# Kernel optimization log

Hardware: AMD Instinct MI355X
Metric: run time of the kernel (lower is better)

## Reference

```python
import jax, jax.numpy as jnp
import numpy as np

N_ING, N_DIR = 100000, 50000
E = 1000000
H, D = 4, 16          # heads, per-head dim
HID = H * D           # 64
LAT, COND = 32, 8
F_ING, F_DIR = 16, 8
OUT_ING = 16


def _han_edge(x_src, x_dst, att_s, att_d, edge_index, n_dst):
    # HANConv per-edge-type attention message passing.
    src, dst = edge_index[0], edge_index[1]
    a = jax.nn.leaky_relu(
        jnp.einsum('nhd,hd->nh', x_src, att_s)[src]
        + jnp.einsum('nhd,hd->nh', x_dst, att_d)[dst],
        negative_slope=0.2)                               # [E, H]
    amax = jax.ops.segment_max(a, dst, num_segments=n_dst)
    ex = jnp.exp(a - amax[dst])
    denom = jax.ops.segment_sum(ex, dst, num_segments=n_dst)
    alpha = ex / (denom[dst] + 1e-16)                     # PyG softmax eps
    out = jax.ops.segment_sum(x_src[src] * alpha[:, :, None], dst,
                              num_segments=n_dst)         # [n_dst, H, D]
    return jax.nn.relu(out.reshape(n_dst, HID))


def _group(outs, q, Wk, bk):
    # HANConv semantic-level attention across edge types.
    s = jnp.stack(outs)                                   # [T, N, HID]
    score = jnp.tanh(s @ Wk + bk).mean(axis=1) @ q        # [T]
    attn = jax.nn.softmax(score)
    return jnp.einsum('t,tnf->nf', attn, s)


def setup_inputs() -> dict:
    key = jax.random.key(0)
    ks = jax.random.split(key, 32)
    def ei(k, n_src, n_dst):
        k1, k2 = jax.random.split(k)
        return jnp.stack([jax.random.randint(k1, (E,), 0, n_src),
                          jax.random.randint(k2, (E,), 0, n_dst)]).astype(jnp.int64)
    s = 0.1
    inp = {
        'x_ing': jax.random.normal(ks[0], (N_ING, F_ING), jnp.float32),
        'x_dir': jax.random.normal(ks[1], (N_DIR, F_DIR), jnp.float32),
        'cond':  jax.random.normal(ks[2], (COND,), jnp.float32),
        'eps':   jax.random.normal(ks[3], (1, LAT), jnp.float32),
        'ei_cooc':     ei(ks[4], N_ING, N_DIR),
        'ei_used':     ei(ks[5], N_ING, N_DIR),
        'ei_contains': ei(ks[6], N_DIR, N_ING),
        'ei_pairs':    ei(ks[7], N_DIR, N_DIR),
        'ei_follows':  ei(ks[8], N_DIR, N_DIR),
        # node-type projections
        'W_pi': jax.random.normal(ks[9],  (F_ING, HID)) * s,
        'b_pi': jnp.zeros((HID,)),
        'W_pd': jax.random.normal(ks[10], (F_DIR, HID)) * s,
        'b_pd': jnp.zeros((HID,)),
        # semantic attention
        'Wk': jax.random.normal(ks[21], (HID, HID)) * s,
        'bk': jnp.zeros((HID,)),
        'q':  jax.random.normal(ks[22], (HID,)) * s,
        # VAE heads (input: 2*HID + COND)
        'W_mu': jax.random.normal(ks[23], (2 * HID + COND, LAT)) * s,
        'b_mu': jnp.zeros((LAT,)),
        'W_lv': jax.random.normal(ks[24], (2 * HID + COND, LAT)) * s,
        'b_lv': jnp.zeros((LAT,)),
        # decoder (fc1 is dead code in the original forward)
        'W_fc3': jax.random.normal(ks[25], (LAT, HID)) * s,
        'b_fc3': jnp.zeros((HID,)),
        'W_fc2': jax.random.normal(ks[26], (HID, OUT_ING)) * s,
        'b_fc2': jnp.zeros((OUT_ING,)),
    }
    for i, name in enumerate(['cooc', 'used', 'contains', 'pairs', 'follows']):
        inp[f'as_{name}'] = jax.random.normal(ks[11 + i], (H, D)) * s
        inp[f'ad_{name}'] = jax.random.normal(ks[16 + i], (H, D)) * s
    return inp


def reference(x_ing, x_dir, cond, eps,
              ei_cooc, ei_used, ei_contains, ei_pairs, ei_follows,
              W_pi, b_pi, W_pd, b_pd,
              as_cooc, ad_cooc, as_used, ad_used, as_contains, ad_contains,
              as_pairs, ad_pairs, as_follows, ad_follows,
              Wk, bk, q, W_mu, b_mu, W_lv, b_lv,
              W_fc3, b_fc3, W_fc2, b_fc2):
    # node-type projections -> [N, H, D]
    h_ing = (x_ing @ W_pi + b_pi).reshape(N_ING, H, D)
    h_dir = (x_dir @ W_pd + b_pd).reshape(N_DIR, H, D)

    o_cooc = _han_edge(h_ing, h_dir, as_cooc, ad_cooc, ei_cooc, N_DIR)
    o_used = _han_edge(h_ing, h_dir, as_used, ad_used, ei_used, N_DIR)
    o_cont = _han_edge(h_dir, h_ing, as_contains, ad_contains, ei_contains, N_ING)
    o_pair = _han_edge(h_dir, h_dir, as_pairs, ad_pairs, ei_pairs, N_DIR)
    o_foll = _han_edge(h_dir, h_dir, as_follows, ad_follows, ei_follows, N_DIR)

    out_ing = _group([o_cont], q, Wk, bk)                       # [N_ING, HID]
    out_dir = _group([o_cooc, o_used, o_pair, o_foll], q, Wk, bk)

    ingre_pool = out_ing.mean(axis=0, keepdims=True)            # [1, HID]
    direc_pool = out_dir.mean(axis=0, keepdims=True)
    graph_repr = jnp.concatenate([ingre_pool, direc_pool, cond[None]], axis=1)

    mu = graph_repr @ W_mu + b_mu
    logvar = graph_repr @ W_lv + b_lv
    z = mu + eps * jnp.exp(0.5 * logvar)

    # decoder: fc1 branch is overwritten in the original; effective path below
    recon = jnp.tanh(jax.nn.relu(z @ W_fc3 + b_fc3) @ W_fc2 + b_fc2)  # [1, OUT_ING]
    return recon, mu, logvar
```

## Files before the change

### kernel.cpp

```cpp
#include <hip/hip_runtime.h>
#include <hip/hip_fp16.h>
#include <math.h>

#define N_ING 100000
#define N_DIR 50000
#define NE    1000000
#define NDST_TOTAL 300000
#define NBUCK 4688
#define BA    64
#define NBK   (5 * BA)
#define I4PT  (NE / 4)
#define PB_ING 384
#define PB_DIR 192
#define LOG2E 1.442695041f

typedef float v2f __attribute__((ext_vector_type(2)));
typedef __attribute__((ext_vector_type(8))) short bf16x8;
typedef __attribute__((ext_vector_type(4))) float f32x4;

__global__ __launch_bounds__(256) void kA_kernel(
    const int* __restrict__ e0, const int* __restrict__ e1,
    const int* __restrict__ e2, const int* __restrict__ e3,
    const int* __restrict__ e4, int* __restrict__ blockcnt,
    const float* __restrict__ x_ing, const float* __restrict__ W_pi,
    const float* __restrict__ b_pi,
    const float* __restrict__ as_cooc, const float* __restrict__ as_used,
    const float* __restrict__ ad_contains,
    unsigned* __restrict__ h8_ing, __half* __restrict__ s_ing,
    const float* __restrict__ x_dir, const float* __restrict__ W_pd,
    const float* __restrict__ b_pd,
    const float* __restrict__ ad_cooc, const float* __restrict__ ad_used,
    const float* __restrict__ as_contains, const float* __restrict__ as_pairs,
    const float* __restrict__ ad_pairs, const float* __restrict__ as_follows,
    const float* __restrict__ ad_follows,
    unsigned* __restrict__ h8_dir, __half* __restrict__ s_dir)
{
    __shared__ int hist[NBUCK];
    __shared__ float sW[16 * 64];
    __shared__ float sbb[64];
    __shared__ float satt[7 * 64];
    __shared__ float sx[4][16];
    __shared__ float srow[4][64];

    const int bid = blockIdx.x;
    const int tid = threadIdx.x;
    if (bid < NBK) {
        const int type = bid / BA, blk = bid % BA;
        const int* ei = type == 0 ? e0 : type == 1 ? e1 : type == 2 ? e2
                      : type == 3 ? e3 : e4;
        const int base = type == 0 ? 0 : type == 1 ? 50000 : type == 2 ? 100000
                       : type == 3 ? 200000 : 250000;
        for (int i = tid; i < NBUCK; i += 256) hist[i] = 0;
        __syncthreads();
        const int4* d4 = (const int4*)(ei + NE);
        for (int i = blk * 256 + tid; i < I4PT; i += BA * 256) {
            int4 d = d4[i];
            atomicAdd(&hist[(base + d.x) >> 6], 1);
            atomicAdd(&hist[(base + d.y) >> 6], 1);
            atomicAdd(&hist[(base + d.z) >> 6], 1);
            atomicAdd(&hist[(base + d.w) >> 6], 1);
        }
        __syncthreads();
        int* row = blockcnt + (size_t)bid * NBUCK;
        for (int i = tid; i < NBUCK; i += 256) row[i] = hist[i];
    } else if (bid < NBK + PB_ING) {
        const int g = tid >> 6, t = tid & 63;
        for (int i = tid; i < 16 * 64; i += 256) sW[i] = W_pi[i];
        if (tid < 64) {
            sbb[tid] = b_pi[tid];
            satt[tid]       = as_cooc[tid] * LOG2E;
            satt[64 + tid]  = as_used[tid] * LOG2E;
            satt[128 + tid] = ad_contains[tid] * LOG2E;
        }
        __syncthreads();
        for (int q = bid - NBK; q < N_ING / 4; q += PB_ING) {
            int n = q * 4 + g;
            if (t < 16) sx[g][t] = x_ing[(size_t)n * 16 + t];
            __syncthreads();
            float s = sbb[t];
#pragma unroll
            for (int i = 0; i < 16; ++i) s += sx[g][i] * sW[i * 64 + t];
            srow[g][t] = s;
            __syncthreads();
            if (t < 16) {
                int w0 = __builtin_amdgcn_cvt_pk_fp8_f32(srow[g][t * 4], srow[g][t * 4 + 1], 0, false);
                int w  = __builtin_amdgcn_cvt_pk_fp8_f32(srow[g][t * 4 + 2], srow[g][t * 4 + 3], w0, true);
                h8_ing[(size_t)n * 16 + t] = (unsigned)w;
            }
            if (t < 12) {
                int slot = t >> 2, hh = t & 3;
                float sc = 0.f;
#pragma unroll
                for (int d = 0; d < 16; ++d)
                    sc += srow[g][hh * 16 + d] * satt[slot * 64 + hh * 16 + d];
                s_ing[(size_t)n * 12 + t] = __float2half(sc);
            }
            __syncthreads();
        }
    } else {
        const int g = tid >> 6, t = tid & 63;
        for (int i = tid; i < 8 * 64; i += 256) sW[i] = W_pd[i];
        if (tid < 64) {
            sbb[tid] = b_pd[tid];
            satt[tid]        = ad_cooc[tid] * LOG2E;
            satt[64  + tid]  = ad_used[tid] * LOG2E;
            satt[128 + tid]  = as_contains[tid] * LOG2E;
            satt[192 + tid]  = as_pairs[tid] * LOG2E;
            satt[256 + tid]  = ad_pairs[tid] * LOG2E;
            satt[320 + tid]  = as_follows[tid] * LOG2E;
            satt[384 + tid]  = ad_follows[tid] * LOG2E;
        }
        __syncthreads();
        for (int q = bid - NBK - PB_ING; q < N_DIR / 4; q += PB_DIR) {
            int n = q * 4 + g;
            if (t < 8) sx[g][t] = x_dir[(size_t)n * 8 + t];
            __syncthreads();
            float s = sbb[t];
#pragma unroll
            for (int i = 0; i < 8; ++i) s += sx[g][i] * sW[i * 64 + t];
            srow[g][t] = s;
            __syncthreads();
            if (t < 16) {
                int w0 = __builtin_amdgcn_cvt_pk_fp8_f32(srow[g][t * 4], srow[g][t * 4 + 1], 0, false);
                int w  = __builtin_amdgcn_cvt_pk_fp8_f32(srow[g][t * 4 + 2], srow[g][t * 4 + 3], w0, true);
                h8_dir[(size_t)n * 16 + t] = (unsigned)w;
            }
            if (t < 28) {
                int slot = t >> 2, hh = t & 3;
                float sc = 0.f;
#pragma unroll
                for (int d = 0; d < 16; ++d)
                    sc += srow[g][hh * 16 + d] * satt[slot * 64 + hh * 16 + d];
                s_dir[(size_t)n * 28 + t] = __float2half(sc);
            }
            __syncthreads();
        }
    }
}

__global__ __launch_bounds__(256) void k2_kernel(
    const int* __restrict__ blockcnt, int* __restrict__ blockbase,
    int* __restrict__ bbase, int* __restrict__ btot, int* __restrict__ cursor)
{
    __shared__ int part[4][64];
    __shared__ int tots[64];
    __shared__ int scn[64];
    __shared__ int bw;
    const int tid = threadIdx.x;
    const int kq = tid >> 6, bl = tid & 63;
    const int b = blockIdx.x * 64 + bl;
    const int K = NBK / 4;
    int ps = 0;
    if (b < NBUCK)
        for (int k = kq * K; k < kq * K + K; ++k)
            ps += blockcnt[(size_t)k * NBUCK + b];
    part[kq][bl] = ps;
    __syncthreads();
    if (tid < 64) {
        int t = part[0][tid] + part[1][tid] + part[2][tid] + part[3][tid];
        tots[tid] = t;
        scn[tid] = t;
    }
    __syncthreads();
    for (int off = 1; off < 64; off <<= 1) {
        int v = 0;
        if (tid < 64 && tid >= off) v = scn[tid - off];
        __syncthreads();
        if (tid < 64) scn[tid] += v;
        __syncthreads();
    }
    if (tid == 63) bw = atomicAdd(cursor, scn[63]);
    __syncthreads();
    if (b < NBUCK) {
        int bs = bw + scn[bl] - tots[bl];
        if (kq == 0) {
            bbase[b] = bs;
            btot[b] = tots[bl];
        }
        int run = bs;
        for (int q = 0; q < kq; ++q) run += part[q][bl];
        for (int k = kq * K; k < kq * K + K; ++k) {
            blockbase[(size_t)k * NBUCK + b] = run;
            run += blockcnt[(size_t)k * NBUCK + b];
        }
    }
}

__global__ __launch_bounds__(256) void k3_kernel(
    const int* __restrict__ e0, const int* __restrict__ e1,
    const int* __restrict__ e2, const int* __restrict__ e3,
    const int* __restrict__ e4, const int* __restrict__ blockbase,
    unsigned* __restrict__ bpair)
{
    __shared__ int cur[NBUCK];
    const int bid = blockIdx.x, tid = threadIdx.x;
    const int type = bid / BA, blk = bid % BA;
    const int* ei = type == 0 ? e0 : type == 1 ? e1 : type == 2 ? e2
                  : type == 3 ? e3 : e4;
    const int base = type == 0 ? 0 : type == 1 ? 50000 : type == 2 ? 100000
                   : type == 3 ? 200000 : 250000;
    const int* row = blockbase + (size_t)bid * NBUCK;
    for (int i = tid; i < NBUCK; i += 256) cur[i] = row[i];
    __syncthreads();
    const int4* s4 = (const int4*)ei;
    const int4* d4 = (const int4*)(ei + NE);
    for (int i = blk * 256 + tid; i < I4PT; i += BA * 256) {
        int4 s = s4[i];
        int4 d = d4[i];
        int g0 = base + d.x, g1 = base + d.y, g2 = base + d.z, g3 = base + d.w;
        int p0 = atomicAdd(&cur[g0 >> 6], 1);
        int p1 = atomicAdd(&cur[g1 >> 6], 1);
        int p2 = atomicAdd(&cur[g2 >> 6], 1);
        int p3 = atomicAdd(&cur[g3 >> 6], 1);
        bpair[p0] = ((unsigned)(g0 & 63) << 17) | (unsigned)s.x;
        bpair[p1] = ((unsigned)(g1 & 63) << 17) | (unsigned)s.y;
        bpair[p2] = ((unsigned)(g2 & 63) << 17) | (unsigned)s.z;
        bpair[p3] = ((unsigned)(g3 & 63) << 17) | (unsigned)s.w;
    }
}

__global__ __launch_bounds__(256) void k4_kernel(
    const unsigned* __restrict__ bpair, const int* __restrict__ bbase,
    const int* __restrict__ btot, int* __restrict__ perm,
    int* __restrict__ start, int* __restrict__ cnt)
{
    __shared__ int h[64], sc[64], cu[64];
    const int b = blockIdx.x, tid = threadIdx.x;
    const int jb = bbase[b], n = btot[b];
    if (tid < 64) h[tid] = 0;
    __syncthreads();
    for (int i = tid; i < n; i += 256)
        atomicAdd(&h[bpair[jb + i] >> 17], 1);
    __syncthreads();
    if (tid == 0) {
        int r = 0;
        for (int i = 0; i < 64; ++i) { sc[i] = r; cu[i] = r; r += h[i]; }
    }
    __syncthreads();
    if (tid < 64) {
        int dg = b * 64 + tid;
        if (dg < NDST_TOTAL) {
            start[dg] = jb + sc[tid];
            cnt[dg] = h[tid];
        }
    }
    for (int i = tid; i < n; i += 256) {
        unsigned p = bpair[jb + i];
        int pos = atomicAdd(&cu[p >> 17], 1);
        perm[jb + pos] = (int)(p & 0x1FFFF);
    }
}

__global__ __launch_bounds__(256) void agg_all_kernel(
    const int* __restrict__ perm, const int* __restrict__ start,
    const int* __restrict__ cnttot,
    const unsigned* __restrict__ h8_ing, const unsigned* __restrict__ h8_dir,
    const __half* __restrict__ s_ing, const __half* __restrict__ s_dir,
    unsigned* __restrict__ rows8,
    float* __restrict__ pool_ing, float* __restrict__ pool_dir)
{
    __shared__ __align__(16) float srow[4][64];
    __shared__ float sred[4][64];
    const int t = threadIdx.x & 63, w = threadIdx.x >> 6;
    const int g  = t >> 4;
    const int l4 = t & 15;
    const int hq = l4 >> 2;

    float p_ing = 0.f;
    float p0 = 0.f, p1 = 0.f, p2 = 0.f, p3 = 0.f;
    const int nwaves = gridDim.x * 4;
    for (int d = blockIdx.x * 4 + w; d < NDST_TOTAL; d += nwaves) {
        int type, ld;
        const __half *ssrc, *sdst;
        const unsigned* hsrc;
        unsigned uss, uds; int soff, doff;
        if (d < 50000)       { type = 0; ld = d;          ssrc = s_ing; uss = 12; soff = 0;  sdst = s_dir; uds = 28; doff = 0;  hsrc = h8_ing; }
        else if (d < 100000) { type = 1; ld = d - 50000;  ssrc = s_ing; uss = 12; soff = 4;  sdst = s_dir; uds = 28; doff = 4;  hsrc = h8_ing; }
        else if (d < 200000) { type = 2; ld = d - 100000; ssrc = s_dir; uss = 28; soff = 8;  sdst = s_ing; uds = 12; doff = 8;  hsrc = h8_dir; }
        else if (d < 250000) { type = 3; ld = d - 200000; ssrc = s_dir; uss = 28; soff = 12; sdst = s_dir; uds = 28; doff = 16; hsrc = h8_dir; }
        else                 { type = 4; ld = d - 250000; ssrc = s_dir; uss = 28; soff = 20; sdst = s_dir; uds = 28; doff = 24; hsrc = h8_dir; }
        float adst = __half2float(sdst[(unsigned)ld * uds + (unsigned)(doff + hq)]);
        const unsigned usoff = (unsigned)(soff + hq);
        int jb = start[d], je = jb + cnttot[d];
        int jl = je - 1;
        float4 acc = make_float4(0.f, 0.f, 0.f, 0.f);
        float dsum = 0.f;
        for (int j = jb; j < je; j += 16) {
            int j0 = j + g, j1 = j + 4 + g, j2 = j + 8 + g, j3 = j + 12 + g;
            bool v0 = j0 < je, v1 = j1 < je, v2 = j2 < je, v3 = j3 < je;
            unsigned s0 = (unsigned)perm[v0 ? j0 : jl];
            unsigned s1 = (unsigned)perm[v1 ? j1 : jl];
            unsigned s2 = (unsigned)perm[v2 ? j2 : jl];
            unsigned s3 = (unsigned)perm[v3 ? j3 : jl];
            float c0 = __half2float(ssrc[s0 * uss + usoff]);
            float c1 = __half2float(ssrc[s1 * uss + usoff]);
            float c2 = __half2float(ssrc[s2 * uss + usoff]);
            float c3 = __half2float(ssrc[s3 * uss + usoff]);
            unsigned u0 = hsrc[s0 * 16u + (unsigned)l4];
            unsigned u1 = hsrc[s1 * 16u + (unsigned)l4];
            unsigned u2 = hsrc[s2 * 16u + (unsigned)l4];
            unsigned u3 = hsrc[s3 * 16u + (unsigned)l4];
            float a0 = c0 + adst; a0 = a0 > 0.f ? a0 : 0.2f * a0;
            float a1 = c1 + adst; a1 = a1 > 0.f ? a1 : 0.2f * a1;
            float a2 = c2 + adst; a2 = a2 > 0.f ? a2 : 0.2f * a2;
            float a3 = c3 + adst; a3 = a3 > 0.f ? a3 : 0.2f * a3;
            float e0 = v0 ? __builtin_amdgcn_exp2f(a0) : 0.f;
            float e1 = v1 ? __builtin_amdgcn_exp2f(a1) : 0.f;
            float e2 = v2 ? __builtin_amdgcn_exp2f(a2) : 0.f;
            float e3 = v3 ? __builtin_amdgcn_exp2f(a3) : 0.f;
            dsum += (e0 + e1) + (e2 + e3);
            v2f lo0 = __builtin_amdgcn_cvt_pk_f32_fp8((int)u0, false);
            v2f hi0 = __builtin_amdgcn_cvt_pk_f32_fp8((int)u0, true);
            v2f lo1 = __builtin_amdgcn_cvt_pk_f32_fp8((int)u1, false);
            v2f hi1 = __builtin_amdgcn_cvt_pk_f32_fp8((int)u1, true);
            v2f lo2 = __builtin_amdgcn_cvt_pk_f32_fp8((int)u2, false);
            v2f hi2 = __builtin_amdgcn_cvt_pk_f32_fp8((int)u2, true);
            v2f lo3 = __builtin_amdgcn_cvt_pk_f32_fp8((int)u3, false);
            v2f hi3 = __builtin_amdgcn_cvt_pk_f32_fp8((int)u3, true);
            acc.x += (lo0.x * e0 + lo1.x * e1) + (lo2.x * e2 + lo3.x * e3);
            acc.y += (lo0.y * e0 + lo1.y * e1) + (lo2.y * e2 + lo3.y * e3);
            acc.z += (hi0.x * e0 + hi1.x * e1) + (hi2.x * e2 + hi3.x * e3);
            acc.w += (hi0.y * e0 + hi1.y * e1) + (hi2.y * e2 + hi3.y * e3);
        }
#pragma unroll
        for (int mask = 16; mask <= 32; mask <<= 1) {
            acc.x += __shfl_xor(acc.x, mask, 64);
            acc.y += __shfl_xor(acc.y, mask, 64);
            acc.z += __shfl_xor(acc.z, mask, 64);
            acc.w += __shfl_xor(acc.w, mask, 64);
            dsum  += __shfl_xor(dsum,  mask, 64);
        }
        float inv = 1.f / (dsum + 1e-16f);
        float4 v4 = make_float4(fmaxf(acc.x * inv, 0.f), fmaxf(acc.y * inv, 0.f),
                                fmaxf(acc.z * inv, 0.f), fmaxf(acc.w * inv, 0.f));
        if (g == 0) *(float4*)&srow[w][l4 * 4] = v4;
        float v = srow[w][t];
        if (type == 2) {
            p_ing += v;
        } else {
            if (type == 0)      p0 += v;
            else if (type == 1) p1 += v;
            else if (type == 3) p2 += v;
            else                p3 += v;
            if (g == 0) {
                unsigned md = (unsigned)(d < 100000 ? d : d - 100000);
                int r0 = __builtin_amdgcn_cvt_pk_fp8_f32(v4.x, v4.y, 0, false);
                int r1 = __builtin_amdgcn_cvt_pk_fp8_f32(v4.z, v4.w, r0, true);
                rows8[md * 16u + (unsigned)l4] = (unsigned)r1;
            }
        }
    }
    float vals[5] = { p_ing, p0, p1, p2, p3 };
    float* outs[5] = { pool_ing, pool_dir, pool_dir + 64, pool_dir + 128,
                       pool_dir + 192 };
    for (int i = 0; i < 5; ++i) {
        __syncthreads();
        sred[w][t] = vals[i];
        __syncthreads();
        if (w == 0)
            atomicAdd(&outs[i][t], sred[0][t] + sred[1][t] + sred[2][t] + sred[3][t]);
    }
}

__global__ __launch_bounds__(256) void sem_kernel(
    const unsigned* __restrict__ rows8, const float* __restrict__ Wk,
    const float* __restrict__ bk, float* __restrict__ sem_dir)
{
    __shared__ float swk[4096];
    __shared__ float ssem[256];
    const int tid = threadIdx.x;
    for (int i = tid; i < 4096; i += 256) swk[i] = Wk[i];
    ssem[tid] = 0.f;
    __syncthreads();

    const int lane = tid & 63, w = tid >> 6;
    const int col = lane & 15, kg = lane >> 4;

    bf16x8 bfr[4][2];
    float biasv[4];
#pragma unroll
    for (int nt = 0; nt < 4; ++nt) {
        biasv[nt] = bk[nt * 16 + col];
#pragma unroll
        for (int ks = 0; ks < 2; ++ks) {
            bf16x8 bb;
#pragma unroll
            for (int j = 0; j < 8; ++j) {
                int k = ks * 32 + kg * 8 + j;
                unsigned u = __builtin_bit_cast(unsigned, swk[k * 64 + nt * 16 + col]);
                u = u + 0x7FFFu + ((u >> 16) & 1u);
                bb[j] = (short)(u >> 16);
            }
            bfr[nt][ks] = bb;
        }
    }

    const int gw = blockIdx.x * 4 + w;
    const int nw = gridDim.x * 4;
    for (int tile = gw; tile < 12500; tile += nw) {
        const int tt = tile / 3125;
        const unsigned* rp = rows8 + (unsigned)(tile * 16 + col) * 16u;
        bf16x8 afr[2];
#pragma unroll
        for (int ks = 0; ks < 2; ++ks) {
            uint2 uu = *(const uint2*)(rp + ks * 8 + kg * 2);
            v2f l0 = __builtin_amdgcn_cvt_pk_f32_fp8((int)uu.x, false);
            v2f h0 = __builtin_amdgcn_cvt_pk_f32_fp8((int)uu.x, true);
            v2f l1 = __builtin_amdgcn_cvt_pk_f32_fp8((int)uu.y, false);
            v2f h1 = __builtin_amdgcn_cvt_pk_f32_fp8((int)uu.y, true);
            bf16x8 aa;
            aa[0] = (short)(__builtin_bit_cast(unsigned, l0.x) >> 16);
            aa[1] = (short)(__builtin_bit_cast(unsigned, l0.y) >> 16);
            aa[2] = (short)(__builtin_bit_cast(unsigned, h0.x) >> 16);
            aa[3] = (short)(__builtin_bit_cast(unsigned, h0.y) >> 16);
            aa[4] = (short)(__builtin_bit_cast(unsigned, l1.x) >> 16);
            aa[5] = (short)(__builtin_bit_cast(unsigned, l1.y) >> 16);
            aa[6] = (short)(__builtin_bit_cast(unsigned, h1.x) >> 16);
            aa[7] = (short)(__builtin_bit_cast(unsigned, h1.y) >> 16);
            afr[ks] = aa;
        }
#pragma unroll
        for (int nt = 0; nt < 4; ++nt) {
            f32x4 acc = {0.f, 0.f, 0.f, 0.f};
            acc = __builtin_amdgcn_mfma_f32_16x16x32_bf16(afr[0], bfr[nt][0], acc, 0, 0, 0);
            acc = __builtin_amdgcn_mfma_f32_16x16x32_bf16(afr[1], bfr[nt][1], acc, 0, 0, 0);
            float s = 0.f;
#pragma unroll
            for (int reg = 0; reg < 4; ++reg) {
                float x = acc[reg] + biasv[nt];
                x = fminf(fmaxf(x, -15.f), 15.f);
                float e = __builtin_amdgcn_exp2f(x * (2.f * LOG2E));
                s += (e - 1.f) * __builtin_amdgcn_rcpf(e + 1.f);
            }
            s += __shfl_xor(s, 16, 64);
            s += __shfl_xor(s, 32, 64);
            if (lane < 16) atomicAdd(&ssem[tt * 64 + nt * 16 + col], s);
        }
    }
    __syncthreads();
    atomicAdd(&sem_dir[tid], ssem[tid]);
}

__global__ __launch_bounds__(64) void final_kernel(
    const float* __restrict__ pool_ing, const float* __restrict__ pool_dir,
    const float* __restrict__ sem_dir, const float* __restrict__ q,
    const float* __restrict__ cond, const float* __restrict__ eps,
    const float* __restrict__ W_mu, const float* __restrict__ b_mu,
    const float* __restrict__ W_lv, const float* __restrict__ b_lv,
    const float* __restrict__ W_fc3, const float* __restrict__ b_fc3,
    const float* __restrict__ W_fc2, const float* __restrict__ b_fc2,
    float* __restrict__ out)
{
    __shared__ float gr[136];
    __shared__ float sc[4], attn[4];
    __shared__ float z[32], hfc[64];
    int t = threadIdx.x;
    if (t < 4) {
        float s = 0.f;
        for (int f = 0; f < 64; ++f)
            s += (sem_dir[t * 64 + f] / (float)N_DIR) * q[f];
        sc[t] = s;
    }
    gr[t] = pool_ing[t] / (float)N_ING;
    __syncthreads();
    if (t == 0) {
        float m = fmaxf(fmaxf(sc[0], sc[1]), fmaxf(sc[2], sc[3]));
        float ssum = 0.f;
        for (int i = 0; i < 4; ++i) { attn[i] = expf(sc[i] - m); ssum += attn[i]; }
        for (int i = 0; i < 4; ++i) attn[i] /= ssum;
    }
    __syncthreads();
    {
        float v = 0.f;
        for (int tt = 0; tt < 4; ++tt)
            v += attn[tt] * (pool_dir[tt * 64 + t] / (float)N_DIR);
        gr[64 + t] = v;
    }
    if (t < 8) gr[128 + t] = cond[t];
    __syncthreads();
    if (t < 32) {
        float m = b_mu[t], lv = b_lv[t];
        for (int i = 0; i < 136; ++i) {
            float g = gr[i];
            m  += g * W_mu[i * 32 + t];
            lv += g * W_lv[i * 32 + t];
        }
        out[16 + t] = m;
        out[48 + t] = lv;
        z[t] = m + eps[t] * expf(0.5f * lv);
    }
    __syncthreads();
    {
        float v = b_fc3[t];
        for (int j = 0; j < 32; ++j) v += z[j] * W_fc3[j * 64 + t];
        hfc[t] = fmaxf(v, 0.f);
    }
    __syncthreads();
    if (t < 16) {
        float v = b_fc2[t];
        for (int f = 0; f < 64; ++f) v += hfc[f] * W_fc2[f * 16 + t];
        out[t] = tanhf(v);
    }
}

extern "C" void kernel_launch(void* const* d_in, const int* in_sizes, int n_in,
                              void* d_out, int out_size, void* d_ws, size_t ws_size,
                              hipStream_t stream) {
    const float* x_ing = (const float*)d_in[0];
    const float* x_dir = (const float*)d_in[1];
    const float* cond  = (const float*)d_in[2];
    const float* eps   = (const float*)d_in[3];
    const int* ei_cooc     = (const int*)d_in[4];
    const int* ei_used     = (const int*)d_in[5];
    const int* ei_contains = (const int*)d_in[6];
    const int* ei_pairs    = (const int*)d_in[7];
    const int* ei_follows  = (const int*)d_in[8];
    const float* W_pi = (const float*)d_in[9];
    const float* b_pi = (const float*)d_in[10];
    const float* W_pd = (const float*)d_in[11];
    const float* b_pd = (const float*)d_in[12];
    const float* Wk   = (const float*)d_in[13];
    const float* bk   = (const float*)d_in[14];
    const float* q    = (const float*)d_in[15];
    const float* W_mu = (const float*)d_in[16];
    const float* b_mu = (const float*)d_in[17];
    const float* W_lv = (const float*)d_in[18];
    const float* b_lv = (const float*)d_in[19];
    const float* W_fc3 = (const float*)d_in[20];
    const float* b_fc3 = (const float*)d_in[21];
    const float* W_fc2 = (const float*)d_in[22];
    const float* b_fc2 = (const float*)d_in[23];
    const float* as_cooc     = (const float*)d_in[24];
    const float* ad_cooc     = (const float*)d_in[25];
    const float* as_used     = (const float*)d_in[26];
    const float* ad_used     = (const float*)d_in[27];
    const float* as_contains = (const float*)d_in[28];
    const float* ad_contains = (const float*)d_in[29];
    const float* as_pairs    = (const float*)d_in[30];
    const float* ad_pairs    = (const float*)d_in[31];
    const float* as_follows  = (const float*)d_in[32];
    const float* ad_follows  = (const float*)d_in[33];

    unsigned* bpair = (unsigned*)d_ws;
    unsigned* h8_ing = bpair + (size_t)5 * NE;
    unsigned* h8_dir = h8_ing + (size_t)N_ING * 16;
    __half* s_ing = (__half*)(h8_dir + (size_t)N_DIR * 16);
    __half* s_dir = s_ing + (size_t)N_ING * 12;
    int*   perm  = (int*)(s_dir + (size_t)N_DIR * 28);
    int*   bbase  = perm + (size_t)5 * NE;
    int*   btot   = bbase + NBUCK;
    int*   start  = btot + NBUCK;
    int*   cnt    = start + NDST_TOTAL;
    int*   cursor = cnt + NDST_TOTAL;
    float* pool_ing = (float*)(cursor + 1);
    float* pool_dir = pool_ing + 64;
    float* sem_dir  = pool_dir + 256;
    unsigned* rows8 = bpair;
    int* blockcnt  = (int*)bpair;
    int* blockbase = (int*)perm;

    hipMemsetAsync(cursor, 0, (1 + 64 + 256 + 256) * sizeof(int), stream);

    kA_kernel<<<NBK + PB_ING + PB_DIR, 256, 0, stream>>>(
        ei_cooc, ei_used, ei_contains, ei_pairs, ei_follows, blockcnt,
        x_ing, W_pi, b_pi, as_cooc, as_used, ad_contains, h8_ing, s_ing,
        x_dir, W_pd, b_pd, ad_cooc, ad_used, as_contains, as_pairs, ad_pairs,
        as_follows, ad_follows, h8_dir, s_dir);

    k2_kernel<<<(NBUCK + 63) / 64, 256, 0, stream>>>(
        blockcnt, blockbase, bbase, btot, cursor);

    k3_kernel<<<NBK, 256, 0, stream>>>(
        ei_cooc, ei_used, ei_contains, ei_pairs, ei_follows, blockbase, bpair);

    k4_kernel<<<NBUCK, 256, 0, stream>>>(bpair, bbase, btot, perm, start, cnt);

    agg_all_kernel<<<2048, 256, 0, stream>>>(
        perm, start, cnt, h8_ing, h8_dir, s_ing, s_dir, rows8,
        pool_ing, pool_dir);

    sem_kernel<<<512, 256, 0, stream>>>(rows8, Wk, bk, sem_dir);

    final_kernel<<<1, 64, 0, stream>>>(
        pool_ing, pool_dir, sem_dir, q, cond, eps,
        W_mu, b_mu, W_lv, b_lv, W_fc3, b_fc3, W_fc2, b_fc2, (float*)d_out);
}
```

Before: 508.4 us.

## Replace two-level bucket sort with global-atomic counting sort by destination

```diff
diff --git a/kernel.cpp b/kernel.cpp
--- a/kernel.cpp
+++ b/kernel.cpp
@@ -6,7 +6,6 @@
 #define N_DIR 50000
 #define NE    1000000
 #define NDST_TOTAL 300000
-#define NBUCK 4688
 #define BA    64
 #define NBK   (5 * BA)
 #define I4PT  (NE / 4)
@@ -21,7 +20,7 @@
 __global__ __launch_bounds__(256) void kA_kernel(
     const int* __restrict__ e0, const int* __restrict__ e1,
     const int* __restrict__ e2, const int* __restrict__ e3,
-    const int* __restrict__ e4, int* __restrict__ blockcnt,
+    const int* __restrict__ e4, int* __restrict__ cnt,
     const float* __restrict__ x_ing, const float* __restrict__ W_pi,
     const float* __restrict__ b_pi,
     const float* __restrict__ as_cooc, const float* __restrict__ as_used,
@@ -35,7 +34,6 @@
     const float* __restrict__ ad_follows,
     unsigned* __restrict__ h8_dir, __half* __restrict__ s_dir)
 {
-    __shared__ int hist[NBUCK];
     __shared__ float sW[16 * 64];
     __shared__ float sbb[64];
     __shared__ float satt[7 * 64];
@@ -50,19 +48,14 @@
                       : type == 3 ? e3 : e4;
         const int base = type == 0 ? 0 : type == 1 ? 50000 : type == 2 ? 100000
                        : type == 3 ? 200000 : 250000;
-        for (int i = tid; i < NBUCK; i += 256) hist[i] = 0;
-        __syncthreads();
         const int4* d4 = (const int4*)(ei + NE);
         for (int i = blk * 256 + tid; i < I4PT; i += BA * 256) {
             int4 d = d4[i];
-            atomicAdd(&hist[(base + d.x) >> 6], 1);
-            atomicAdd(&hist[(base + d.y) >> 6], 1);
-            atomicAdd(&hist[(base + d.z) >> 6], 1);
-            atomicAdd(&hist[(base + d.w) >> 6], 1);
-        }
-        __syncthreads();
-        int* row = blockcnt + (size_t)bid * NBUCK;
-        for (int i = tid; i < NBUCK; i += 256) row[i] = hist[i];
+            atomicAdd(&cnt[base + d.x], 1);
+            atomicAdd(&cnt[base + d.y], 1);
+            atomicAdd(&cnt[base + d.z], 1);
+            atomicAdd(&cnt[base + d.w], 1);
+        }
     } else if (bid < NBK + PB_ING) {
         const int g = tid >> 6, t = tid & 63;
         for (int i = tid; i < 16 * 64; i += 256) sW[i] = W_pi[i];
@@ -138,116 +131,77 @@
     }
 }
 
-__global__ __launch_bounds__(256) void k2_kernel(
-    const int* __restrict__ blockcnt, int* __restrict__ blockbase,
-    int* __restrict__ bbase, int* __restrict__ btot, int* __restrict__ cursor)
+__global__ __launch_bounds__(256) void scan_kernel(
+    const int* __restrict__ cnt, int* __restrict__ start,
+    int* __restrict__ cur, int* __restrict__ cursor)
 {
-    __shared__ int part[4][64];
-    __shared__ int tots[64];
-    __shared__ int scn[64];
-    __shared__ int bw;
+    __shared__ int tsum[256];
+    __shared__ int bbase_s;
     const int tid = threadIdx.x;
-    const int kq = tid >> 6, bl = tid & 63;
-    const int b = blockIdx.x * 64 + bl;
-    const int K = NBK / 4;
-    int ps = 0;
-    if (b < NBUCK)
-        for (int k = kq * K; k < kq * K + K; ++k)
-            ps += blockcnt[(size_t)k * NBUCK + b];
-    part[kq][bl] = ps;
-    __syncthreads();
-    if (tid < 64) {
-        int t = part[0][tid] + part[1][tid] + part[2][tid] + part[3][tid];
-        tots[tid] = t;
-        scn[tid] = t;
-    }
-    __syncthreads();
-    for (int off = 1; off < 64; off <<= 1) {
-        int v = 0;
-        if (tid < 64 && tid >= off) v = scn[tid - off];
+    const int base = blockIdx.x * 4096 + tid * 16;
+    const bool val = base < NDST_TOTAL;
+    int v[16];
+    int s = 0;
+    if (val) {
+        const int4* c4 = (const int4*)(cnt + base);
+#pragma unroll
+        for (int q = 0; q < 4; ++q) {
+            int4 c = c4[q];
+            v[q * 4 + 0] = c.x; v[q * 4 + 1] = c.y;
+            v[q * 4 + 2] = c.z; v[q * 4 + 3] = c.w;
+            s += c.x + c.y + c.z + c.w;
+        }
+    } else {
+#pragma unroll
+        for (int k = 0; k < 16; ++k) v[k] = 0;
+    }
+    tsum[tid] = s;
+    __syncthreads();
+    for (int off = 1; off < 256; off <<= 1) {
+        int t2 = 0;
+        if (tid >= off) t2 = tsum[tid - off];
         __syncthreads();
-        if (tid < 64) scn[tid] += v;
+        tsum[tid] += t2;
         __syncthreads();
     }
-    if (tid == 63) bw = atomicAdd(cursor, scn[63]);
-    __syncthreads();
-    if (b < NBUCK) {
-        int bs = bw + scn[bl] - tots[bl];
-        if (kq == 0) {
-            bbase[b] = bs;
-            btot[b] = tots[bl];
-        }
-        int run = bs;
-        for (int q = 0; q < kq; ++q) run += part[q][bl];
-        for (int k = kq * K; k < kq * K + K; ++k) {
-            blockbase[(size_t)k * NBUCK + b] = run;
-            run += blockcnt[(size_t)k * NBUCK + b];
-        }
-    }
-}
-
-__global__ __launch_bounds__(256) void k3_kernel(
+    if (tid == 255) bbase_s = atomicAdd(cursor, tsum[255]);
+    __syncthreads();
+    if (val) {
+        int run = bbase_s + tsum[tid] - s;
+#pragma unroll
+        for (int k = 0; k < 16; ++k) {
+            start[base + k] = run;
+            cur[base + k] = run;
+            run += v[k];
+        }
+    }
+}
+
+__global__ __launch_bounds__(256) void scatter_kernel(
     const int* __restrict__ e0, const int* __restrict__ e1,
     const int* __restrict__ e2, const int* __restrict__ e3,
-    const int* __restrict__ e4, const int* __restrict__ blockbase,
-    unsigned* __restrict__ bpair)
+    const int* __restrict__ e4, int* __restrict__ cur,
+    int* __restrict__ perm)
 {
-    __shared__ int cur[NBUCK];
     const int bid = blockIdx.x, tid = threadIdx.x;
     const int type = bid / BA, blk = bid % BA;
     const int* ei = type == 0 ? e0 : type == 1 ? e1 : type == 2 ? e2
                   : type == 3 ? e3 : e4;
     const int base = type == 0 ? 0 : type == 1 ? 50000 : type == 2 ? 100000
                    : type == 3 ? 200000 : 250000;
-    const int* row = blockbase + (size_t)bid * NBUCK;
-    for (int i = tid; i < NBUCK; i += 256) cur[i] = row[i];
-    __syncthreads();
     const int4* s4 = (const int4*)ei;
     const int4* d4 = (const int4*)(ei + NE);
     for (int i = blk * 256 + tid; i < I4PT; i += BA * 256) {
         int4 s = s4[i];
         int4 d = d4[i];
-        int g0 = base + d.x, g1 = base + d.y, g2 = base + d.z, g3 = base + d.w;
-        int p0 = atomicAdd(&cur[g0 >> 6], 1);
-        int p1 = atomicAdd(&cur[g1 >> 6], 1);
-        int p2 = atomicAdd(&cur[g2 >> 6], 1);
-        int p3 = atomicAdd(&cur[g3 >> 6], 1);
-        bpair[p0] = ((unsigned)(g0 & 63) << 17) | (unsigned)s.x;
-        bpair[p1] = ((unsigned)(g1 & 63) << 17) | (unsigned)s.y;
-        bpair[p2] = ((unsigned)(g2 & 63) << 17) | (unsigned)s.z;
-        bpair[p3] = ((unsigned)(g3 & 63) << 17) | (unsigned)s.w;
-    }
-}
-
-__global__ __launch_bounds__(256) void k4_kernel(
-    const unsigned* __restrict__ bpair, const int* __restrict__ bbase,
-    const int* __restrict__ btot, int* __restrict__ perm,
-    int* __restrict__ start, int* __restrict__ cnt)
-{
-    __shared__ int h[64], sc[64], cu[64];
-    const int b = blockIdx.x, tid = threadIdx.x;
-    const int jb = bbase[b], n = btot[b];
-    if (tid < 64) h[tid] = 0;
-    __syncthreads();
-    for (int i = tid; i < n; i += 256)
-        atomicAdd(&h[bpair[jb + i] >> 17], 1);
-    __syncthreads();
-    if (tid == 0) {
-        int r = 0;
-        for (int i = 0; i < 64; ++i) { sc[i] = r; cu[i] = r; r += h[i]; }
-    }
-    __syncthreads();
-    if (tid < 64) {
-        int dg = b * 64 + tid;
-        if (dg < NDST_TOTAL) {
-            start[dg] = jb + sc[tid];
-            cnt[dg] = h[tid];
-        }
-    }
-    for (int i = tid; i < n; i += 256) {
-        unsigned p = bpair[jb + i];
-        int pos = atomicAdd(&cu[p >> 17], 1);
-        perm[jb + pos] = (int)(p & 0x1FFFF);
+        int p0 = atomicAdd(&cur[base + d.x], 1);
+        int p1 = atomicAdd(&cur[base + d.y], 1);
+        int p2 = atomicAdd(&cur[base + d.z], 1);
+        int p3 = atomicAdd(&cur[base + d.w], 1);
+        perm[p0] = s.x;
+        perm[p1] = s.y;
+        perm[p2] = s.z;
+        perm[p3] = s.w;
     }
 }
 
@@ -541,39 +495,34 @@
     const float* as_follows  = (const float*)d_in[32];
     const float* ad_follows  = (const float*)d_in[33];
 
-    unsigned* bpair = (unsigned*)d_ws;
-    unsigned* h8_ing = bpair + (size_t)5 * NE;
+    int* perm = (int*)d_ws;
+    unsigned* h8_ing = (unsigned*)(perm + (size_t)5 * NE);
     unsigned* h8_dir = h8_ing + (size_t)N_ING * 16;
     __half* s_ing = (__half*)(h8_dir + (size_t)N_DIR * 16);
     __half* s_dir = s_ing + (size_t)N_ING * 12;
-    int*   perm  = (int*)(s_dir + (size_t)N_DIR * 28);
-    int*   bbase  = perm + (size_t)5 * NE;
-    int*   btot   = bbase + NBUCK;
-    int*   start  = btot + NBUCK;
-    int*   cnt    = start + NDST_TOTAL;
-    int*   cursor = cnt + NDST_TOTAL;
+    unsigned* rows8 = (unsigned*)(s_dir + (size_t)N_DIR * 28);
+    int* cur    = (int*)(rows8 + (size_t)200000 * 16);
+    int* start  = cur + NDST_TOTAL;
+    int* cnt    = start + NDST_TOTAL;
+    int* cursor = cnt + NDST_TOTAL;
     float* pool_ing = (float*)(cursor + 1);
     float* pool_dir = pool_ing + 64;
     float* sem_dir  = pool_dir + 256;
-    unsigned* rows8 = bpair;
-    int* blockcnt  = (int*)bpair;
-    int* blockbase = (int*)perm;
-
-    hipMemsetAsync(cursor, 0, (1 + 64 + 256 + 256) * sizeof(int), stream);
+
+    hipMemsetAsync(cnt, 0, (NDST_TOTAL + 1 + 64 + 256 + 256) * sizeof(int),
+                   stream);
 
     kA_kernel<<<NBK + PB_ING + PB_DIR, 256, 0, stream>>>(
-        ei_cooc, ei_used, ei_contains, ei_pairs, ei_follows, blockcnt,
+        ei_cooc, ei_used, ei_contains, ei_pairs, ei_follows, cnt,
         x_ing, W_pi, b_pi, as_cooc, as_used, ad_contains, h8_ing, s_ing,
         x_dir, W_pd, b_pd, ad_cooc, ad_used, as_contains, as_pairs, ad_pairs,
         as_follows, ad_follows, h8_dir, s_dir);
 
-    k2_kernel<<<(NBUCK + 63) / 64, 256, 0, stream>>>(
-        blockcnt, blockbase, bbase, btot, cursor);
-
-    k3_kernel<<<NBK, 256, 0, stream>>>(
-        ei_cooc, ei_used, ei_contains, ei_pairs, ei_follows, blockbase, bpair);
-
-    k4_kernel<<<NBUCK, 256, 0, stream>>>(bpair, bbase, btot, perm, start, cnt);
+    scan_kernel<<<(NDST_TOTAL + 4095) / 4096, 256, 0, stream>>>(
+        cnt, start, cur, cursor);
+
+    scatter_kernel<<<NBK, 256, 0, stream>>>(
+        ei_cooc, ei_used, ei_contains, ei_pairs, ei_follows, cur, perm);
 
     agg_all_kernel<<<2048, 256, 0, stream>>>(
         perm, start, cnt, h8_ing, h8_dir, s_ing, s_dir, rows8,
```

New measurement: 996.5 us. 1.96x slower.

## Fuse bucket-local sort into aggregation kernel using shared-memory permutation

Applied to the files above, without the earlier changes.

```diff
diff --git a/kernel.cpp b/kernel.cpp
--- a/kernel.cpp
+++ b/kernel.cpp
@@ -12,6 +12,7 @@
 #define I4PT  (NE / 4)
 #define PB_ING 384
 #define PB_DIR 192
+#define CAP   2048
 #define LOG2E 1.442695041f
 
 typedef float v2f __attribute__((ext_vector_type(2)));
@@ -219,57 +220,60 @@
     }
 }
 
-__global__ __launch_bounds__(256) void k4_kernel(
+__global__ __launch_bounds__(256) void agg_all_kernel(
     const unsigned* __restrict__ bpair, const int* __restrict__ bbase,
-    const int* __restrict__ btot, int* __restrict__ perm,
-    int* __restrict__ start, int* __restrict__ cnt)
-{
-    __shared__ int h[64], sc[64], cu[64];
-    const int b = blockIdx.x, tid = threadIdx.x;
-    const int jb = bbase[b], n = btot[b];
-    if (tid < 64) h[tid] = 0;
-    __syncthreads();
-    for (int i = tid; i < n; i += 256)
-        atomicAdd(&h[bpair[jb + i] >> 17], 1);
-    __syncthreads();
-    if (tid == 0) {
-        int r = 0;
-        for (int i = 0; i < 64; ++i) { sc[i] = r; cu[i] = r; r += h[i]; }
-    }
-    __syncthreads();
-    if (tid < 64) {
-        int dg = b * 64 + tid;
-        if (dg < NDST_TOTAL) {
-            start[dg] = jb + sc[tid];
-            cnt[dg] = h[tid];
-        }
-    }
-    for (int i = tid; i < n; i += 256) {
-        unsigned p = bpair[jb + i];
-        int pos = atomicAdd(&cu[p >> 17], 1);
-        perm[jb + pos] = (int)(p & 0x1FFFF);
-    }
-}
-
-__global__ __launch_bounds__(256) void agg_all_kernel(
-    const int* __restrict__ perm, const int* __restrict__ start,
-    const int* __restrict__ cnttot,
+    const int* __restrict__ btot,
     const unsigned* __restrict__ h8_ing, const unsigned* __restrict__ h8_dir,
     const __half* __restrict__ s_ing, const __half* __restrict__ s_dir,
     unsigned* __restrict__ rows8,
     float* __restrict__ pool_ing, float* __restrict__ pool_dir)
 {
+    __shared__ unsigned sbp[CAP];
+    __shared__ unsigned lperm[CAP];
+    __shared__ int h[64], sc[64], cu[64];
     __shared__ __align__(16) float srow[4][64];
     __shared__ float sred[4][64];
-    const int t = threadIdx.x & 63, w = threadIdx.x >> 6;
+    const int tid = threadIdx.x;
+    const int t = tid & 63, w = tid >> 6;
     const int g  = t >> 4;
     const int l4 = t & 15;
     const int hq = l4 >> 2;
+    const int b = blockIdx.x;
+    const int jbg = bbase[b], n = btot[b];
+
+    if (tid < 64) h[tid] = 0;
+    __syncthreads();
+    const bool fast = (n <= CAP);
+    if (fast) {
+        for (int i = tid; i < n; i += 256) {
+            unsigned p = bpair[jbg + i];
+            sbp[i] = p;
+            atomicAdd(&h[p >> 17], 1);
+        }
+    } else {
+        for (int i = tid; i < n; i += 256)
+            atomicAdd(&h[bpair[jbg + i] >> 17], 1);
+    }
+    __syncthreads();
+    if (tid == 0) {
+        int r = 0;
+        for (int i = 0; i < 64; ++i) { sc[i] = r; cu[i] = r; r += h[i]; }
+    }
+    __syncthreads();
+    if (fast) {
+        for (int i = tid; i < n; i += 256) {
+            unsigned p = sbp[i];
+            int pos = atomicAdd(&cu[p >> 17], 1);
+            lperm[pos] = p & 0x1FFFFu;
+        }
+    }
+    __syncthreads();
 
     float p_ing = 0.f;
     float p0 = 0.f, p1 = 0.f, p2 = 0.f, p3 = 0.f;
-    const int nwaves = gridDim.x * 4;
-    for (int d = blockIdx.x * 4 + w; d < NDST_TOTAL; d += nwaves) {
+    for (int dl = w; dl < 64; dl += 4) {
+        const int d = b * 64 + dl;
+        if (d >= NDST_TOTAL) break;
         int type, ld;
         const __half *ssrc, *sdst;
         const unsigned* hsrc;
@@ -281,46 +285,65 @@
         else                 { type = 4; ld = d - 250000; ssrc = s_dir; uss = 28; soff = 20; sdst = s_dir; uds = 28; doff = 24; hsrc = h8_dir; }
         float adst = __half2float(sdst[(unsigned)ld * uds + (unsigned)(doff + hq)]);
         const unsigned usoff = (unsigned)(soff + hq);
-        int jb = start[d], je = jb + cnttot[d];
-        int jl = je - 1;
         float4 acc = make_float4(0.f, 0.f, 0.f, 0.f);
         float dsum = 0.f;
-        for (int j = jb; j < je; j += 16) {
-            int j0 = j + g, j1 = j + 4 + g, j2 = j + 8 + g, j3 = j + 12 + g;
-            bool v0 = j0 < je, v1 = j1 < je, v2 = j2 < je, v3 = j3 < je;
-            unsigned s0 = (unsigned)perm[v0 ? j0 : jl];
-            unsigned s1 = (unsigned)perm[v1 ? j1 : jl];
-            unsigned s2 = (unsigned)perm[v2 ? j2 : jl];
-            unsigned s3 = (unsigned)perm[v3 ? j3 : jl];
-            float c0 = __half2float(ssrc[s0 * uss + usoff]);
-            float c1 = __half2float(ssrc[s1 * uss + usoff]);
-            float c2 = __half2float(ssrc[s2 * uss + usoff]);
-            float c3 = __half2float(ssrc[s3 * uss + usoff]);
-            unsigned u0 = hsrc[s0 * 16u + (unsigned)l4];
-            unsigned u1 = hsrc[s1 * 16u + (unsigned)l4];
-            unsigned u2 = hsrc[s2 * 16u + (unsigned)l4];
-            unsigned u3 = hsrc[s3 * 16u + (unsigned)l4];
-            float a0 = c0 + adst; a0 = a0 > 0.f ? a0 : 0.2f * a0;
-            float a1 = c1 + adst; a1 = a1 > 0.f ? a1 : 0.2f * a1;
-            float a2 = c2 + adst; a2 = a2 > 0.f ? a2 : 0.2f * a2;
-            float a3 = c3 + adst; a3 = a3 > 0.f ? a3 : 0.2f * a3;
-            float e0 = v0 ? __builtin_amdgcn_exp2f(a0) : 0.f;
-            float e1 = v1 ? __builtin_amdgcn_exp2f(a1) : 0.f;
-            float e2 = v2 ? __builtin_amdgcn_exp2f(a2) : 0.f;
-            float e3 = v3 ? __builtin_amdgcn_exp2f(a3) : 0.f;
-            dsum += (e0 + e1) + (e2 + e3);
-            v2f lo0 = __builtin_amdgcn_cvt_pk_f32_fp8((int)u0, false);
-            v2f hi0 = __builtin_amdgcn_cvt_pk_f32_fp8((int)u0, true);
-            v2f lo1 = __builtin_amdgcn_cvt_pk_f32_fp8((int)u1, false);
-            v2f hi1 = __builtin_amdgcn_cvt_pk_f32_fp8((int)u1, true);
-            v2f lo2 = __builtin_amdgcn_cvt_pk_f32_fp8((int)u2, false);
-            v2f hi2 = __builtin_amdgcn_cvt_pk_f32_fp8((int)u2, true);
-            v2f lo3 = __builtin_amdgcn_cvt_pk_f32_fp8((int)u3, false);
-            v2f hi3 = __builtin_amdgcn_cvt_pk_f32_fp8((int)u3, true);
-            acc.x += (lo0.x * e0 + lo1.x * e1) + (lo2.x * e2 + lo3.x * e3);
-            acc.y += (lo0.y * e0 + lo1.y * e1) + (lo2.y * e2 + lo3.y * e3);
-            acc.z += (hi0.x * e0 + hi1.x * e1) + (hi2.x * e2 + hi3.x * e3);
-            acc.w += (hi0.y * e0 + hi1.y * e1) + (hi2.y * e2 + hi3.y * e3);
+        if (fast) {
+            const int jb = sc[dl], je = jb + h[dl];
+            const int jl = je - 1;
+            for (int j = jb; j < je; j += 16) {
+                int j0 = j + g, j1 = j + 4 + g, j2 = j + 8 + g, j3 = j + 12 + g;
+                bool v0 = j0 < je, v1 = j1 < je, v2 = j2 < je, v3 = j3 < je;
+                unsigned s0 = lperm[v0 ? j0 : jl];
+                unsigned s1 = lperm[v1 ? j1 : jl];
+                unsigned s2 = lperm[v2 ? j2 : jl];
+                unsigned s3 = lperm[v3 ? j3 : jl];
+                float c0 = __half2float(ssrc[s0 * uss + usoff]);
+                float c1 = __half2float(ssrc[s1 * uss + usoff]);
+                float c2 = __half2float(ssrc[s2 * uss + usoff]);
+                float c3 = __half2float(ssrc[s3 * uss + usoff]);
+                unsigned u0 = hsrc[s0 * 16u + (unsigned)l4];
+                unsigned u1 = hsrc[s1 * 16u + (unsigned)l4];
+                unsigned u2 = hsrc[s2 * 16u + (unsigned)l4];
+                unsigned u3 = hsrc[s3 * 16u + (unsigned)l4];
+                float a0 = c0 + adst; a0 = a0 > 0.f ? a0 : 0.2f * a0;
+                float a1 = c1 + adst; a1 = a1 > 0.f ? a1 : 0.2f * a1;
+                float a2 = c2 + adst; a2 = a2 > 0.f ? a2 : 0.2f * a2;
+                float a3 = c3 + adst; a3 = a3 > 0.f ? a3 : 0.2f * a3;
+                float e0 = v0 ? __builtin_amdgcn_exp2f(a0) : 0.f;
+                float e1 = v1 ? __builtin_amdgcn_exp2f(a1) : 0.f;
+                float e2 = v2 ? __builtin_amdgcn_exp2f(a2) : 0.f;
+                float e3 = v3 ? __builtin_amdgcn_exp2f(a3) : 0.f;
+                dsum += (e0 + e1) + (e2 + e3);
+                v2f lo0 = __builtin_amdgcn_cvt_pk_f32_fp8((int)u0, false);
+                v2f hi0 = __builtin_amdgcn_cvt_pk_f32_fp8((int)u0, true);
+                v2f lo1 = __builtin_amdgcn_cvt_pk_f32_fp8((int)u1, false);
+                v2f hi1 = __builtin_amdgcn_cvt_pk_f32_fp8((int)u1, true);
+                v2f lo2 = __builtin_amdgcn_cvt_pk_f32_fp8((int)u2, false);
+                v2f hi2 = __builtin_amdgcn_cvt_pk_f32_fp8((int)u2, true);
+                v2f lo3 = __builtin_amdgcn_cvt_pk_f32_fp8((int)u3, false);
+                v2f hi3 = __builtin_amdgcn_cvt_pk_f32_fp8((int)u3, true);
+                acc.x += (lo0.x * e0 + lo1.x * e1) + (lo2.x * e2 + lo3.x * e3);
+                acc.y += (lo0.y * e0 + lo1.y * e1) + (lo2.y * e2 + lo3.y * e3);
+                acc.z += (hi0.x * e0 + hi1.x * e1) + (hi2.x * e2 + hi3.x * e3);
+                acc.w += (hi0.y * e0 + hi1.y * e1) + (hi2.y * e2 + hi3.y * e3);
+            }
+        } else {
+            for (int j = g; j < n; j += 4) {
+                unsigned p = bpair[jbg + j];
+                bool m = (p >> 17) == (unsigned)dl;
+                unsigned s0 = p & 0x1FFFFu;
+                float c0 = __half2float(ssrc[s0 * uss + usoff]);
+                unsigned u0 = hsrc[s0 * 16u + (unsigned)l4];
+                float a0 = c0 + adst; a0 = a0 > 0.f ? a0 : 0.2f * a0;
+                float e0 = m ? __builtin_amdgcn_exp2f(a0) : 0.f;
+                dsum += e0;
+                v2f lo0 = __builtin_amdgcn_cvt_pk_f32_fp8((int)u0, false);
+                v2f hi0 = __builtin_amdgcn_cvt_pk_f32_fp8((int)u0, true);
+                acc.x += lo0.x * e0;
+                acc.y += lo0.y * e0;
+                acc.z += hi0.x * e0;
+                acc.w += hi0.y * e0;
+            }
         }
 #pragma unroll
         for (int mask = 16; mask <= 32; mask <<= 1) {
@@ -546,18 +569,15 @@
     unsigned* h8_dir = h8_ing + (size_t)N_ING * 16;
     __half* s_ing = (__half*)(h8_dir + (size_t)N_DIR * 16);
     __half* s_dir = s_ing + (size_t)N_ING * 12;
-    int*   perm  = (int*)(s_dir + (size_t)N_DIR * 28);
-    int*   bbase  = perm + (size_t)5 * NE;
-    int*   btot   = bbase + NBUCK;
-    int*   start  = btot + NBUCK;
-    int*   cnt    = start + NDST_TOTAL;
-    int*   cursor = cnt + NDST_TOTAL;
+    unsigned* rows8 = (unsigned*)(s_dir + (size_t)N_DIR * 28);
+    int* blockcnt  = (int*)rows8;
+    int* blockbase = blockcnt + (size_t)NBK * NBUCK;
+    int* bbase  = (int*)(rows8 + (size_t)200000 * 16);
+    int* btot   = bbase + NBUCK;
+    int* cursor = btot + NBUCK;
     float* pool_ing = (float*)(cursor + 1);
     float* pool_dir = pool_ing + 64;
     float* sem_dir  = pool_dir + 256;
-    unsigned* rows8 = bpair;
-    int* blockcnt  = (int*)bpair;
-    int* blockbase = (int*)perm;
 
     hipMemsetAsync(cursor, 0, (1 + 64 + 256 + 256) * sizeof(int), stream);
 
@@ -573,10 +593,8 @@
     k3_kernel<<<NBK, 256, 0, stream>>>(
         ei_cooc, ei_used, ei_contains, ei_pairs, ei_follows, blockbase, bpair);
 
-    k4_kernel<<<NBUCK, 256, 0, stream>>>(bpair, bbase, btot, perm, start, cnt);
-
-    agg_all_kernel<<<2048, 256, 0, stream>>>(
-        perm, start, cnt, h8_ing, h8_dir, s_ing, s_dir, rows8,
+    agg_all_kernel<<<NBUCK, 256, 0, stream>>>(
+        bpair, bbase, btot, h8_ing, h8_dir, s_ing, s_dir, rows8,
         pool_ing, pool_dir);
 
     sem_kernel<<<512, 256, 0, stream>>>(rows8, Wk, bk, sem_dir);
```

New measurement: 512.1 us. No clear change (+0.7%).
